# Kernel tuning notes

Hardware: AMD Instinct MI355X
Metric: run time of the kernel (lower is better)

## Reference

```python
import jax, jax.numpy as jnp
import numpy as np

B, T, I, R, O = 32, 1000, 3, 2048, 3
SPECTRAL_RADIUS = 0.95
SPARSITY = 0.02
INPUT_SCALING = 100.0
INPUT_WEIGHTS_SCALING = 0.01
NOISE_LEVEL = 0.01


def _make_reservoir(size, spectral_radius, sparsity, scale, rng):
    # mirrors EchoStateNetwork.generate_reservoir
    W = ((rng.random((size, size)) - 0.5) * scale).astype(np.float32)
    mask = rng.random((size, size)) > sparsity
    W[mask] = 0.0
    eig = np.linalg.eigvals(W.astype(np.float64))
    actual_sr = np.max(np.abs(eig))
    W = W * np.float32(spectral_radius / actual_sr)
    return jnp.asarray(W)


def setup_inputs() -> dict:
    key = jax.random.key(0)
    k1, k2, k3, k4 = jax.random.split(key, 4)
    x = jax.random.normal(k1, (B, T, I), dtype=jnp.float32)
    input_weights = jax.random.normal(k2, (R, I), dtype=jnp.float32) * INPUT_SCALING
    reservoir_weights = _make_reservoir(R, SPECTRAL_RADIUS, SPARSITY,
                                        INPUT_WEIGHTS_SCALING,
                                        np.random.default_rng(0))
    output_weights = jax.random.normal(k3, (O, R), dtype=jnp.float32)
    # torch draws noise once (outside the time loop) and reuses it every step
    noise = jax.random.normal(k4, (B, R), dtype=jnp.float32) * NOISE_LEVEL
    return {"x": x, "input_weights": input_weights,
            "reservoir_weights": reservoir_weights,
            "output_weights": output_weights, "noise": noise}


def reference(x, input_weights, reservoir_weights, output_weights, noise):
    batch = x.shape[0]
    res = reservoir_weights.shape[0]
    init = jnp.zeros((batch, res), dtype=x.dtype)

    def step(state, x_t):  # x_t: [B, I]
        new = jnp.tanh(x_t @ input_weights.T + state @ reservoir_weights.T + noise)
        return new, new

    last, states = jax.lax.scan(step, init, jnp.swapaxes(x, 0, 1))  # states: [T,B,R]
    states = jnp.swapaxes(states, 0, 1)  # [B, T, R]
    outputs = last @ output_weights.T    # [B, O]
    return outputs, states
```

## Files before the change

kernel.cpp:

```cpp
#include <hip/hip_runtime.h>
#include <cstddef>

#define B_DIM 32
#define T_DIM 1000
#define I_DIM 3
#define R_DIM 2048
#define O_DIM 3
#define NBLK 256
#define ROWS 8
#define NTHR 512
#define KCH 128
#define NCH 8

__global__ __launch_bounds__(NTHR, 2) void esn_persist(
    const float* __restrict__ x,
    const float* __restrict__ Win,
    const float* __restrict__ Wres,
    const float* __restrict__ Wout,
    const float* __restrict__ noise,
    float* __restrict__ states,
    float* __restrict__ out,
    int* __restrict__ flags)
{
  __shared__ float cross[4][64];

  const int tid   = threadIdx.x;
  const int blk   = blockIdx.x;
  const int r0    = blk * ROWS;
  const int h     = tid >> 8;
  const int wv    = tid >> 6;
  const int wv4   = wv & 3;
  const int lane  = tid & 63;
  const int bbase = wv4 * 8;

  const int ob  = bbase + (lane >> 3);
  const int orr = r0 + (lane & 7);

  float w0 = 0.f, w1 = 0.f, w2 = 0.f, nz = 0.f;
  if (h == 0) {
    w0 = Win[orr * I_DIM + 0];
    w1 = Win[orr * I_DIM + 1];
    w2 = Win[orr * I_DIM + 2];
    nz = noise[(size_t)ob * R_DIM + orr];
  }

  const int klb = h * 1024 + lane * 2;
  const float* wp[8];
  const float* sp0[8];
#pragma unroll
  for (int r = 0; r < 8; ++r) wp[r] = Wres + (size_t)(r0 + r) * R_DIM + klb;
#pragma unroll
  for (int j = 0; j < 8; ++j)
    sp0[j] = states + (size_t)(bbase + j) * T_DIM * R_DIM + klb;

#define LOADC(kc, SF, WF)                                                      \
  {                                                                            \
    _Pragma("unroll")                                                          \
    for (int j = 0; j < 8; ++j)                                                \
      SF[j] = *(const float2*)(sp0[j] + soff + (kc) * KCH);                    \
    _Pragma("unroll")                                                          \
    for (int r = 0; r < 8; ++r)                                                \
      WF[r] = *(const float2*)(wp[r] + (kc) * KCH);                            \
  }

#define FMAC(SF, WF)                                                           \
  {                                                                            \
    _Pragma("unroll")                                                          \
    for (int j = 0; j < 8; ++j) {                                              \
      _Pragma("unroll")                                                        \
      for (int r = 0; r < 8; ++r)                                              \
        acc[j * 8 + r] += WF[r].x * SF[j].x + WF[r].y * SF[j].y;               \
    }                                                                          \
  }

#pragma unroll 1
  for (int t = 0; t < T_DIM; ++t) {
    float x0 = 0.f, x1 = 0.f, x2 = 0.f;
    if (h == 0) {
      const float* xp = &x[((size_t)ob * T_DIM + t) * I_DIM];
      x0 = xp[0]; x1 = xp[1]; x2 = xp[2];
    }

    float acc[64];
#pragma unroll
    for (int i = 0; i < 64; ++i) acc[i] = 0.f;

    if (t > 0) {
      const size_t soff = (size_t)(t - 1) * R_DIM;
      float2 sA[8], wA[8], sB[8], wB[8];
      LOADC(0, sA, wA);
#pragma unroll
      for (int kc = 0; kc < NCH; kc += 2) {
        LOADC(kc + 1, sB, wB);
        FMAC(sA, wA);
        if (kc + 2 < NCH) LOADC(kc + 2, sA, wA);
        FMAC(sB, wB);
      }
    }

#pragma unroll
    for (int m = 32; m >= 1; m >>= 1) {
#pragma unroll
      for (int i = 0; i < m; ++i) {
        const bool hh = (lane & m) != 0;
        const float mine = hh ? acc[i] : acc[i + m];
        const float keep = hh ? acc[i + m] : acc[i];
        acc[i] = keep + __shfl_xor(mine, m, 64);
      }
    }

    if (h == 1) cross[wv4][lane] = acc[0];
    __syncthreads();
    if (h == 0) {
      const float val =
          tanhf(x0 * w0 + x1 * w1 + x2 * w2 + nz + acc[0] + cross[wv4][lane]);
      __hip_atomic_store(&states[((size_t)ob * T_DIM + t) * R_DIM + orr], val,
                         __ATOMIC_RELAXED, __HIP_MEMORY_SCOPE_AGENT);
    }
    __syncthreads();

    if (tid == 0)
      __hip_atomic_store(&flags[blk], t + 1, __ATOMIC_RELAXED,
                         __HIP_MEMORY_SCOPE_AGENT);
    if (wv == 0 && (t + 1 < T_DIM || blk == 0)) {
      const int target = t + 1;
      int guard = 0;
      for (;;) {
        const int v0 = __hip_atomic_load(&flags[lane], __ATOMIC_RELAXED,
                                         __HIP_MEMORY_SCOPE_AGENT);
        const int v1 = __hip_atomic_load(&flags[lane + 64], __ATOMIC_RELAXED,
                                         __HIP_MEMORY_SCOPE_AGENT);
        const int v2 = __hip_atomic_load(&flags[lane + 128], __ATOMIC_RELAXED,
                                         __HIP_MEMORY_SCOPE_AGENT);
        const int v3 = __hip_atomic_load(&flags[lane + 192], __ATOMIC_RELAXED,
                                         __HIP_MEMORY_SCOPE_AGENT);
        const bool ok =
            (v0 >= target) && (v1 >= target) && (v2 >= target) && (v3 >= target);
        if (__all(ok)) break;
        if (++guard > (1 << 22)) break;
        __builtin_amdgcn_s_sleep(1);
      }
    }
    __builtin_amdgcn_fence(__ATOMIC_ACQUIRE, "workgroup");
    __syncthreads();
  }

  if (blk == 0) {
#pragma unroll 1
    for (int pi = 0; pi < 12; ++pi) {
      const int p = wv * 12 + pi;
      const int b = p / 3, o = p % 3;
      const float* sp = &states[((size_t)b * T_DIM + (T_DIM - 1)) * R_DIM];
      const float* wq = &Wout[(size_t)o * R_DIM];
      float a = 0.f;
#pragma unroll
      for (int j = 0; j < 8; ++j) {
        const int rr = j * 256 + lane * 4;
        const float4 s = *(const float4*)&sp[rr];
        const float4 w = *(const float4*)&wq[rr];
        a += s.x * w.x + s.y * w.y + s.z * w.z + s.w * w.w;
      }
#pragma unroll
      for (int m = 32; m >= 1; m >>= 1) a += __shfl_xor(a, m, 64);
      if (lane == 0) out[(size_t)b * O_DIM + o] = a;
    }
  }
}

extern "C" void kernel_launch(void* const* d_in, const int* in_sizes, int n_in,
                              void* d_out, int out_size, void* d_ws, size_t ws_size,
                              hipStream_t stream) {
  const float* x     = (const float*)d_in[0];
  const float* Win   = (const float*)d_in[1];
  const float* Wres  = (const float*)d_in[2];
  const float* Wout  = (const float*)d_in[3];
  const float* noise = (const float*)d_in[4];

  float* out    = (float*)d_out;
  float* states = out + B_DIM * O_DIM;
  int* flags    = (int*)d_ws;

  esn_persist<<<NBLK, NTHR, 0, stream>>>(x, Win, Wres, Wout, noise,
                                         states, out, flags);
}
```

Before: 18.47 ms.

## Replace per-step global barrier with per-chunk producer flag waits

Drops the all-block barrier at the end of each timestep. Each wave now polls only the flags of the 16 producer blocks that own each k-chunk it is about to read, in two halves, so loading and multiply-adding can start before the whole grid has finished. The chunk order is rotated per block group to spread out which producers are polled and read first. Only block 0 still waits on every block, at the end, before computing the output projection. The cost is more flag polling per step and a heavier reliance on the relaxed-atomic ordering being correct.

```diff
diff --git a/kernel.cpp b/kernel.cpp
--- a/kernel.cpp
+++ b/kernel.cpp
@@ -33,6 +33,8 @@
   const int lane  = tid & 63;
   const int bbase = wv4 * 8;
 
+  const int rot = (blk >> 4) & 7;
+
   const int ob  = bbase + (lane >> 3);
   const int orr = r0 + (lane & 7);
 
@@ -43,6 +45,9 @@
     w2 = Win[orr * I_DIM + 2];
     nz = noise[(size_t)ob * R_DIM + orr];
   }
+
+  const int wf_coff = lane >> 4;
+  const int wf_p    = lane & 15;
 
   const int klb = h * 1024 + lane * 2;
   const float* wp[8];
@@ -73,6 +78,21 @@
     }                                                                          \
   }
 
+#define WAITF(cbase, target)                                                   \
+  {                                                                            \
+    const int c    = ((cbase) + wf_coff) & 7;                                  \
+    const int pidx = h * 128 + c * 16 + wf_p;                                  \
+    int guard = 0;                                                             \
+    for (;;) {                                                                 \
+      const int v = __hip_atomic_load(&flags[pidx], __ATOMIC_RELAXED,          \
+                                      __HIP_MEMORY_SCOPE_AGENT);               \
+      if (__all(v >= (target))) break;                                         \
+      if (++guard > (1 << 22)) break;                     \
+      __builtin_amdgcn_s_sleep(1);                                             \
+    }                                                                          \
+    __builtin_amdgcn_fence(__ATOMIC_ACQUIRE, "workgroup");                     \
+  }
+
 #pragma unroll 1
   for (int t = 0; t < T_DIM; ++t) {
     float x0 = 0.f, x1 = 0.f, x2 = 0.f;
@@ -87,15 +107,22 @@
 
     if (t > 0) {
       const size_t soff = (size_t)(t - 1) * R_DIM;
+      const int c0 = rot, c1 = (rot + 1) & 7, c2 = (rot + 2) & 7,
+                c3 = (rot + 3) & 7, c4 = (rot + 4) & 7, c5 = (rot + 5) & 7,
+                c6 = (rot + 6) & 7, c7 = (rot + 7) & 7;
       float2 sA[8], wA[8], sB[8], wB[8];
-      LOADC(0, sA, wA);
-#pragma unroll
-      for (int kc = 0; kc < NCH; kc += 2) {
-        LOADC(kc + 1, sB, wB);
-        FMAC(sA, wA);
-        if (kc + 2 < NCH) LOADC(kc + 2, sA, wA);
-        FMAC(sB, wB);
-      }
+      WAITF(rot, t);
+      LOADC(c0, sA, wA);
+      LOADC(c1, sB, wB);
+      FMAC(sA, wA); LOADC(c2, sA, wA);
+      FMAC(sB, wB); LOADC(c3, sB, wB);
+      WAITF(rot + 4, t);
+      FMAC(sA, wA); LOADC(c4, sA, wA);
+      FMAC(sB, wB); LOADC(c5, sB, wB);
+      FMAC(sA, wA); LOADC(c6, sA, wA);
+      FMAC(sB, wB); LOADC(c7, sB, wB);
+      FMAC(sA, wA);
+      FMAC(sB, wB);
     }
 
 #pragma unroll
@@ -118,24 +145,23 @@
                          __ATOMIC_RELAXED, __HIP_MEMORY_SCOPE_AGENT);
     }
     __syncthreads();
-
     if (tid == 0)
       __hip_atomic_store(&flags[blk], t + 1, __ATOMIC_RELAXED,
                          __HIP_MEMORY_SCOPE_AGENT);
-    if (wv == 0 && (t + 1 < T_DIM || blk == 0)) {
-      const int target = t + 1;
+  }
+
+  if (blk == 0) {
+    if (wv == 0) {
       int guard = 0;
       for (;;) {
-        const int v0 = __hip_atomic_load(&flags[lane], __ATOMIC_RELAXED,
-                                         __HIP_MEMORY_SCOPE_AGENT);
-        const int v1 = __hip_atomic_load(&flags[lane + 64], __ATOMIC_RELAXED,
-                                         __HIP_MEMORY_SCOPE_AGENT);
-        const int v2 = __hip_atomic_load(&flags[lane + 128], __ATOMIC_RELAXED,
-                                         __HIP_MEMORY_SCOPE_AGENT);
-        const int v3 = __hip_atomic_load(&flags[lane + 192], __ATOMIC_RELAXED,
-                                         __HIP_MEMORY_SCOPE_AGENT);
-        const bool ok =
-            (v0 >= target) && (v1 >= target) && (v2 >= target) && (v3 >= target);
+        bool ok = true;
+#pragma unroll
+        for (int j = 0; j < NBLK / 64; ++j) {
+          const int v = __hip_atomic_load(&flags[lane + j * 64],
+                                          __ATOMIC_RELAXED,
+                                          __HIP_MEMORY_SCOPE_AGENT);
+          ok = ok && (v >= T_DIM);
+        }
         if (__all(ok)) break;
         if (++guard > (1 << 22)) break;
         __builtin_amdgcn_s_sleep(1);
@@ -143,9 +169,6 @@
     }
     __builtin_amdgcn_fence(__ATOMIC_ACQUIRE, "workgroup");
     __syncthreads();
-  }
-
-  if (blk == 0) {
 #pragma unroll 1
     for (int pi = 0; pi < 12; ++pi) {
       const int p = wv * 12 + pi;
```

Measured after the change: 31.22 ms. 69.0% more time.
